# Kernel optimization log

Measured on AMD Instinct MI355X. Metric: run time of the kernel, lower is better.

Reference implementation:

```python
import jax, jax.numpy as jnp
import numpy as np

N, E, C, EC, L = 50000, 600000, 128, 16, 4
LN_EPS = 1e-5


def setup_inputs() -> dict:
    key = jax.random.key(0)
    ks = jax.random.split(key, 10)
    return {
        "x": jax.random.normal(ks[0], (N, C), jnp.float32),
        "edge_attr": jax.random.normal(ks[1], (E, EC), jnp.float32),
        "We": jax.random.normal(ks[2], (EC, C), jnp.float32) / np.sqrt(EC).astype(np.float32),
        "be": jnp.zeros((C,), jnp.float32),
        "W1": jax.random.normal(ks[3], (L, C, C), jnp.float32) / np.sqrt(C).astype(np.float32),
        "b1": jnp.zeros((L, C), jnp.float32),
        "W2": jax.random.normal(ks[4], (L, C, C), jnp.float32) / np.sqrt(C).astype(np.float32),
        "b2": jnp.zeros((L, C), jnp.float32),
        "gamma": jnp.ones((L, C), jnp.float32),
        "beta": jnp.zeros((L, C), jnp.float32),
        "edge_index": jax.random.randint(ks[5], (2, E), 0, N, dtype=jnp.int32),
    }


def reference(x, edge_attr, We, be, W1, b1, W2, b2, gamma, beta, edge_index):
    src = edge_index[0]  # x_j (message source)
    dst = edge_index[1]  # aggregation target
    # lin_edge: Linear + SiLU, shared across layers
    ea = jax.nn.silu(edge_attr @ We + be)  # [E, C]
    n = x.shape[0]
    for l in range(L):
        # GINEConv message: ReLU(x_j + edge_attr), scatter-sum to target nodes
        msg = jax.nn.relu(x[src] + ea)                       # [E, C]
        agg = jax.ops.segment_sum(msg, dst, num_segments=n)  # [N, C]
        h = x + agg  # (1 + eps) * x + agg, eps = 0
        # GINEConv nn: Linear -> SiLU -> Linear
        h = jax.nn.silu(h @ W1[l] + b1[l]) @ W2[l] + b2[l]
        # residual + LayerNorm
        y = x + h
        mu = y.mean(-1, keepdims=True)
        var = y.var(-1, keepdims=True)
        x = (y - mu) * jax.lax.rsqrt(var + LN_EPS) * gamma[l] + beta[l]
    return x
```

## Files before the change

kernel.cpp:

```cpp
#include <hip/hip_runtime.h>

#define NN 50000
#define EE 600000
#define CC 128
#define ECC 16
#define LL 4
#define LN_EPS 1e-5f
#define MTILE 80
#define PADC 136
#define YSTR 132

typedef float f32x4 __attribute__((ext_vector_type(4)));
typedef short bf16x8 __attribute__((ext_vector_type(8)));

static __device__ __forceinline__ float bf2f(unsigned short u) {
  union { unsigned int i; float f; } v; v.i = ((unsigned int)u) << 16; return v.f;
}
static __device__ __forceinline__ unsigned short f2bf(float f) {
  union { float f; unsigned int i; } v; v.f = f;
  unsigned int b = v.i + 0x7FFFu + ((v.i >> 16) & 1u);
  return (unsigned short)(b >> 16);
}
static __device__ __forceinline__ unsigned pk2bf(float lo, float hi) {
  unsigned r;
  asm("v_cvt_pk_bf16_f32 %0, %1, %2" : "=v"(r) : "v"(lo), "v"(hi));
  return r;
}
static __device__ __forceinline__ float silu_f(float v) {
  return v * __builtin_amdgcn_rcpf(1.f + __expf(-v));
}


__global__ void count_kernel(const int* __restrict__ dst, int* __restrict__ counts, int E) {
  int e = blockIdx.x * blockDim.x + threadIdx.x;
  if (e < E) atomicAdd(&counts[dst[e]], 1);
}

__global__ __launch_bounds__(1024) void scan1_kernel(const int* __restrict__ counts,
                                                     int* __restrict__ bsum, int n) {
  __shared__ int wsum[16];
  const int tid = threadIdx.x, lane = tid & 63, wv = tid >> 6;
  const int i = blockIdx.x * 1024 + tid;
  int s = (i < n) ? counts[i] : 0;
  #pragma unroll
  for (int off = 1; off < 64; off <<= 1) s += __shfl_xor(s, off);
  if (lane == 0) wsum[wv] = s;
  __syncthreads();
  if (tid == 0) {
    int t = 0;
    #pragma unroll
    for (int j = 0; j < 16; ++j) t += wsum[j];
    bsum[blockIdx.x] = t;
  }
}

__global__ void scan2_kernel(const int* __restrict__ bsum, int* __restrict__ boff, int nb) {
  const int lane = threadIdx.x;
  int v = (lane < nb) ? bsum[lane] : 0;
  int incl = v;
  #pragma unroll
  for (int off = 1; off < 64; off <<= 1) {
    int t = __shfl_up(incl, off);
    if (lane >= off) incl += t;
  }
  if (lane < nb) boff[lane] = incl - v;
}

__global__ __launch_bounds__(1024) void scan3_kernel(const int* __restrict__ counts,
                                                     const int* __restrict__ boff,
                                                     int* __restrict__ rowptr, int n) {
  __shared__ int wsum[16];
  const int tid = threadIdx.x, lane = tid & 63, wv = tid >> 6;
  const int i = blockIdx.x * 1024 + tid;
  const int v = (i < n) ? counts[i] : 0;
  int incl = v;
  #pragma unroll
  for (int off = 1; off < 64; off <<= 1) {
    int t = __shfl_up(incl, off);
    if (lane >= off) incl += t;
  }
  if (lane == 63) wsum[wv] = incl;
  __syncthreads();
  if (wv == 0) {
    int vv = (lane < 16) ? wsum[lane] : 0;
    int vi = vv;
    #pragma unroll
    for (int off = 1; off < 16; off <<= 1) {
      int t = __shfl_up(vi, off);
      if (lane >= off) vi += t;
    }
    if (lane < 16) wsum[lane] = vi - vv;
  }
  __syncthreads();
  if (i < n) rowptr[i + 1] = boff[blockIdx.x] + wsum[wv] + incl;
  if (i == 0) rowptr[0] = 0;
}

__global__ void fill_kernel(const int* __restrict__ src, const int* __restrict__ dst,
                            const int* __restrict__ rowptr, int* __restrict__ cursor,
                            int* __restrict__ eidx, int* __restrict__ esrc, int E) {
  int e = blockIdx.x * blockDim.x + threadIdx.x;
  if (e < E) {
    const int d = dst[e];
    const int pos = rowptr[d] + atomicAdd(&cursor[d], 1);
    eidx[pos] = e;
    esrc[pos] = src[e];
  }
}


__global__ __launch_bounds__(256) void xconv_kernel(const float* __restrict__ x,
                                                    unsigned short* __restrict__ xb) {
  const int t = blockIdx.x * 256 + threadIdx.x;
  if (t >= NN * CC / 8) return;
  const float4 a = ((const float4*)x)[t * 2];
  const float4 b = ((const float4*)x)[t * 2 + 1];
  uint4 o;
  o.x = pk2bf(a.x, a.y);
  o.y = pk2bf(a.z, a.w);
  o.z = pk2bf(b.x, b.y);
  o.w = pk2bf(b.z, b.w);
  ((uint4*)xb)[t] = o;
}


__global__ void webconv_kernel(const float* __restrict__ We, unsigned short* __restrict__ webf) {
  const int t = blockIdx.x * blockDim.x + threadIdx.x;
  if (t >= 8 * 64 * 8) return;
  const int j = t & 7, l = (t >> 3) & 63, cg = t >> 9;
  const int k = (l >> 4) * 8 + j, c = cg * 16 + (l & 15);
  webf[t] = (k < 16) ? f2bf(We[k * CC + c]) : (unsigned short)0;
}


__global__ __launch_bounds__(256) void ea_kernel(const float* __restrict__ edge_attr,
                                                 const unsigned short* __restrict__ webf,
                                                 const float* __restrict__ be,
                                                 const int* __restrict__ eidx,
                                                 unsigned short* __restrict__ ea) {
  __shared__ float er[64][20];
  __shared__ unsigned short eaT[64 * 132];
  const int tid = threadIdx.x;
  const int lane = tid & 63, wv = tid >> 6;

  bf16x8 bw[8];
  #pragma unroll
  for (int cg = 0; cg < 8; ++cg)
    bw[cg] = *(const bf16x8*)(webf + cg * 512 + lane * 8);
  float bev[8];
  #pragma unroll
  for (int cg = 0; cg < 8; ++cg) bev[cg] = be[cg * 16 + (lane & 15)];

  const int base = blockIdx.x * 64;
  {
    const int r = tid >> 2, q = tid & 3;
    const int e = eidx[base + r];
    *(float4*)(&er[r][q * 4]) = *(const float4*)(edge_attr + (size_t)e * ECC + q * 4);
  }
  __syncthreads();

  const int arow = wv * 16 + (lane & 15);
  const int ko = lane >> 4;
  union { unsigned short u[8]; unsigned v32[4]; bf16x8 v; } afu;
  if (ko < 2) {
    const float* ep = &er[arow][ko * 8];
    afu.v32[0] = pk2bf(ep[0], ep[1]);
    afu.v32[1] = pk2bf(ep[2], ep[3]);
    afu.v32[2] = pk2bf(ep[4], ep[5]);
    afu.v32[3] = pk2bf(ep[6], ep[7]);
  } else {
    #pragma unroll
    for (int j = 0; j < 4; ++j) afu.v32[j] = 0;
  }

  f32x4 acc[8];
  #pragma unroll
  for (int cg = 0; cg < 8; ++cg) {
    acc[cg] = (f32x4)0.f;
    acc[cg] = __builtin_amdgcn_mfma_f32_16x16x32_bf16(afu.v, bw[cg], acc[cg], 0, 0, 0);
  }

  const int rl0 = wv * 16 + ko * 4;
  const int cb = lane & 15;
  #pragma unroll
  for (int cg = 0; cg < 8; cg += 2)
    #pragma unroll
    for (int r = 0; r < 4; ++r) {
      const float v0 = silu_f(acc[cg][r] + bev[cg]);
      const float v1 = silu_f(acc[cg + 1][r] + bev[cg + 1]);
      const unsigned pk = pk2bf(v0, v1);
      unsigned short* rp = &eaT[(rl0 + r) * 132 + cb];
      rp[cg * 16]       = (unsigned short)pk;
      rp[(cg + 1) * 16] = (unsigned short)(pk >> 16);
    }
  __syncthreads();

  uint4* eg = (uint4*)(ea + (size_t)base * CC);
  #pragma unroll
  for (int k = 0; k < 4; ++k) {
    const int u = tid + k * 256;
    const int row = u >> 4, ch = u & 15;
    eg[u] = *(const uint4*)(&eaT[row * 132 + ch * 8]);
  }
}


__global__ __launch_bounds__(128) void wconv_kernel(const float* __restrict__ W1,
                                                    const float* __restrict__ W2,
                                                    unsigned short* __restrict__ wt) {
  const int b = blockIdx.x;
  const int c = b & (CC - 1);
  const int mat = (b >> 7) & 1;
  const int l = b >> 8;
  const float* W = (mat ? W2 : W1) + (size_t)l * CC * CC;
  unsigned short* o = wt + ((size_t)l * 2 + mat) * CC * CC + (size_t)c * CC;
  const int k = threadIdx.x;
  o[k] = f2bf(W[(size_t)k * CC + c]);
}


__global__ __launch_bounds__(256) void agg4_kernel(const unsigned short* __restrict__ xb,
                                                   unsigned short* __restrict__ h_out,
                                                   const unsigned short* __restrict__ ea,
                                                   const int* __restrict__ rowptr,
                                                   const int* __restrict__ esrc) {
  const int tid = threadIdx.x;
  const int lane = tid & 63;
  const int half = lane >> 5;
  const int l32 = lane & 31;
  const int c0 = l32 * 4;
  const int wv = tid >> 6;
  const int n = blockIdx.x * 4 + wv;

  const int p0 = rowptr[n], p1 = rowptr[n + 1];
  float a0 = 0.f, a1 = 0.f, a2 = 0.f, a3 = 0.f;

  int p = p0 + half;
  for (; p + 6 < p1; p += 8) {
    const int s0 = esrc[p], s1 = esrc[p + 2], s2 = esrc[p + 4], s3 = esrc[p + 6];
    const uint2 x0 = *(const uint2*)(xb + (size_t)s0 * CC + c0);
    const uint2 x1 = *(const uint2*)(xb + (size_t)s1 * CC + c0);
    const uint2 x2 = *(const uint2*)(xb + (size_t)s2 * CC + c0);
    const uint2 x3 = *(const uint2*)(xb + (size_t)s3 * CC + c0);
    const uint2 e0 = *(const uint2*)(ea + (size_t)p * CC + c0);
    const uint2 e1 = *(const uint2*)(ea + (size_t)(p + 2) * CC + c0);
    const uint2 e2 = *(const uint2*)(ea + (size_t)(p + 4) * CC + c0);
    const uint2 e3 = *(const uint2*)(ea + (size_t)(p + 6) * CC + c0);
    a0 += fmaxf(bf2f((unsigned short)x0.x) + bf2f((unsigned short)e0.x), 0.f)
        + fmaxf(bf2f((unsigned short)x1.x) + bf2f((unsigned short)e1.x), 0.f)
        + fmaxf(bf2f((unsigned short)x2.x) + bf2f((unsigned short)e2.x), 0.f)
        + fmaxf(bf2f((unsigned short)x3.x) + bf2f((unsigned short)e3.x), 0.f);
    a1 += fmaxf(bf2f((unsigned short)(x0.x >> 16)) + bf2f((unsigned short)(e0.x >> 16)), 0.f)
        + fmaxf(bf2f((unsigned short)(x1.x >> 16)) + bf2f((unsigned short)(e1.x >> 16)), 0.f)
        + fmaxf(bf2f((unsigned short)(x2.x >> 16)) + bf2f((unsigned short)(e2.x >> 16)), 0.f)
        + fmaxf(bf2f((unsigned short)(x3.x >> 16)) + bf2f((unsigned short)(e3.x >> 16)), 0.f);
    a2 += fmaxf(bf2f((unsigned short)x0.y) + bf2f((unsigned short)e0.y), 0.f)
        + fmaxf(bf2f((unsigned short)x1.y) + bf2f((unsigned short)e1.y), 0.f)
        + fmaxf(bf2f((unsigned short)x2.y) + bf2f((unsigned short)e2.y), 0.f)
        + fmaxf(bf2f((unsigned short)x3.y) + bf2f((unsigned short)e3.y), 0.f);
    a3 += fmaxf(bf2f((unsigned short)(x0.y >> 16)) + bf2f((unsigned short)(e0.y >> 16)), 0.f)
        + fmaxf(bf2f((unsigned short)(x1.y >> 16)) + bf2f((unsigned short)(e1.y >> 16)), 0.f)
        + fmaxf(bf2f((unsigned short)(x2.y >> 16)) + bf2f((unsigned short)(e2.y >> 16)), 0.f)
        + fmaxf(bf2f((unsigned short)(x3.y >> 16)) + bf2f((unsigned short)(e3.y >> 16)), 0.f);
  }
  for (; p < p1; p += 2) {
    const int s0 = esrc[p];
    const uint2 x0 = *(const uint2*)(xb + (size_t)s0 * CC + c0);
    const uint2 e0 = *(const uint2*)(ea + (size_t)p * CC + c0);
    a0 += fmaxf(bf2f((unsigned short)x0.x) + bf2f((unsigned short)e0.x), 0.f);
    a1 += fmaxf(bf2f((unsigned short)(x0.x >> 16)) + bf2f((unsigned short)(e0.x >> 16)), 0.f);
    a2 += fmaxf(bf2f((unsigned short)x0.y) + bf2f((unsigned short)e0.y), 0.f);
    a3 += fmaxf(bf2f((unsigned short)(x0.y >> 16)) + bf2f((unsigned short)(e0.y >> 16)), 0.f);
  }

  a0 += __shfl_xor(a0, 32);
  a1 += __shfl_xor(a1, 32);
  a2 += __shfl_xor(a2, 32);
  a3 += __shfl_xor(a3, 32);

  if (half == 0) {
    const uint2 xs = *(const uint2*)(xb + (size_t)n * CC + c0);
    uint2 pk;
    pk.x = pk2bf(bf2f((unsigned short)xs.x) + a0, bf2f((unsigned short)(xs.x >> 16)) + a1);
    pk.y = pk2bf(bf2f((unsigned short)xs.y) + a2, bf2f((unsigned short)(xs.y >> 16)) + a3);
    *(uint2*)(h_out + (size_t)n * CC + c0) = pk;
  }
}


__global__ __launch_bounds__(256) void agg_fb_kernel(const unsigned short* __restrict__ xb,
                                                     unsigned short* __restrict__ h_out,
                                                     const float* __restrict__ edge_attr,
                                                     const float* __restrict__ We,
                                                     const float* __restrict__ be,
                                                     const int* __restrict__ rowptr,
                                                     const int* __restrict__ eidx,
                                                     const int* __restrict__ esrc) {
  const int tid = threadIdx.x;
  const int c = tid & (CC - 1);
  const int g = tid >> 7;
  const int n = blockIdx.x * 2 + g;

  float wec[ECC];
  #pragma unroll
  for (int k = 0; k < ECC; ++k) wec[k] = We[k * CC + c];
  const float bev = be[c];

  const int p0 = rowptr[n], p1 = rowptr[n + 1];
  float acc = 0.f;
  for (int p = p0; p < p1; ++p) {
    const int e0 = eidx[p];
    const int s0 = esrc[p];
    const float4* ar0 = (const float4*)(edge_attr + (size_t)e0 * ECC);
    const float4 a0 = ar0[0], a1 = ar0[1], a2 = ar0[2], a3 = ar0[3];
    float v0 = bev
      + a0.x*wec[0]  + a0.y*wec[1]  + a0.z*wec[2]  + a0.w*wec[3]
      + a1.x*wec[4]  + a1.y*wec[5]  + a1.z*wec[6]  + a1.w*wec[7]
      + a2.x*wec[8]  + a2.y*wec[9]  + a2.z*wec[10] + a2.w*wec[11]
      + a3.x*wec[12] + a3.y*wec[13] + a3.z*wec[14] + a3.w*wec[15];
    acc += fmaxf(bf2f(xb[(size_t)s0 * CC + c]) + silu_f(v0), 0.f);
  }
  h_out[(size_t)n * CC + c] = f2bf(bf2f(xb[(size_t)n * CC + c]) + acc);
}


template <int FINAL>
__global__ __launch_bounds__(256) void mlp_kernel(unsigned short* xb,
                                                  const unsigned short* __restrict__ hbuf,
                                                  const unsigned short* __restrict__ wt1,
                                                  const unsigned short* __restrict__ wt2,
                                                  const float* __restrict__ b1,
                                                  const float* __restrict__ b2,
                                                  const float* __restrict__ gamma,
                                                  const float* __restrict__ beta,
                                                  float* __restrict__ out) {
  __shared__ __align__(16) char smem[MTILE * PADC * 2 * 2];
  unsigned short* hA = (unsigned short*)smem;
  unsigned short* tA = (unsigned short*)(smem + MTILE * PADC * 2);
  float* yS = (float*)smem;
  __shared__ float red[MTILE][4][2];

  const int tid = threadIdx.x;
  const int lane = tid & 63;
  const int wv = tid >> 6;
  const int node0 = blockIdx.x * MTILE;
  const int colq = lane & 15;
  const int krow = lane >> 4;
  const int colb = wv * 32;

  for (int idx = tid; idx < MTILE * 16; idx += 256) {
    const int row = idx >> 4, ch = idx & 15;
    *(uint4*)(&hA[row * PADC + ch * 8]) =
        *(const uint4*)(hbuf + (size_t)(node0 + row) * CC + ch * 8);
  }
  __syncthreads();

  bf16x8 bw[2][4];
  #pragma unroll
  for (int n2 = 0; n2 < 2; ++n2)
    #pragma unroll
    for (int kk = 0; kk < 4; ++kk)
      bw[n2][kk] = *(const bf16x8*)(wt1 + (size_t)(colb + n2 * 16 + colq) * CC + kk * 32 + krow * 8);

  f32x4 acc[5][2];
  #pragma unroll
  for (int m = 0; m < 5; ++m) { acc[m][0] = (f32x4)0.f; acc[m][1] = (f32x4)0.f; }

  #pragma unroll
  for (int m = 0; m < 5; ++m)
    #pragma unroll
    for (int kk = 0; kk < 4; ++kk) {
      const bf16x8 a = *(const bf16x8*)(&hA[(m * 16 + colq) * PADC + kk * 32 + krow * 8]);
      acc[m][0] = __builtin_amdgcn_mfma_f32_16x16x32_bf16(a, bw[0][kk], acc[m][0], 0, 0, 0);
      acc[m][1] = __builtin_amdgcn_mfma_f32_16x16x32_bf16(a, bw[1][kk], acc[m][1], 0, 0, 0);
    }

  const float b1v0 = b1[colb + colq], b1v1 = b1[colb + 16 + colq];
  #pragma unroll
  for (int m = 0; m < 5; ++m)
    #pragma unroll
    for (int r = 0; r < 4; ++r) {
      const int row = m * 16 + krow * 4 + r;
      const unsigned pk = pk2bf(silu_f(acc[m][0][r] + b1v0), silu_f(acc[m][1][r] + b1v1));
      tA[row * PADC + colb + colq]      = (unsigned short)pk;
      tA[row * PADC + colb + 16 + colq] = (unsigned short)(pk >> 16);
    }
  __syncthreads();

  #pragma unroll
  for (int n2 = 0; n2 < 2; ++n2)
    #pragma unroll
    for (int kk = 0; kk < 4; ++kk)
      bw[n2][kk] = *(const bf16x8*)(wt2 + (size_t)(colb + n2 * 16 + colq) * CC + kk * 32 + krow * 8);

  f32x4 acc2[5][2];
  #pragma unroll
  for (int m = 0; m < 5; ++m) { acc2[m][0] = (f32x4)0.f; acc2[m][1] = (f32x4)0.f; }

  #pragma unroll
  for (int m = 0; m < 5; ++m)
    #pragma unroll
    for (int kk = 0; kk < 4; ++kk) {
      const bf16x8 a = *(const bf16x8*)(&tA[(m * 16 + colq) * PADC + kk * 32 + krow * 8]);
      acc2[m][0] = __builtin_amdgcn_mfma_f32_16x16x32_bf16(a, bw[0][kk], acc2[m][0], 0, 0, 0);
      acc2[m][1] = __builtin_amdgcn_mfma_f32_16x16x32_bf16(a, bw[1][kk], acc2[m][1], 0, 0, 0);
    }

  const float b2v0 = b2[colb + colq], b2v1 = b2[colb + 16 + colq];
  float yv[5][2][4];
  #pragma unroll
  for (int m = 0; m < 5; ++m)
    #pragma unroll
    for (int r = 0; r < 4; ++r) {
      const int row = m * 16 + krow * 4 + r;
      yv[m][0][r] = acc2[m][0][r] + b2v0 + bf2f(xb[(size_t)(node0 + row) * CC + colb + colq]);
      yv[m][1][r] = acc2[m][1][r] + b2v1 + bf2f(xb[(size_t)(node0 + row) * CC + colb + 16 + colq]);
    }

  #pragma unroll
  for (int m = 0; m < 5; ++m)
    #pragma unroll
    for (int r = 0; r < 4; ++r) {
      float s = yv[m][0][r] + yv[m][1][r];
      float s2 = yv[m][0][r] * yv[m][0][r] + yv[m][1][r] * yv[m][1][r];
      #pragma unroll
      for (int off = 1; off < 16; off <<= 1) {
        s  += __shfl_xor(s, off);
        s2 += __shfl_xor(s2, off);
      }
      if (colq == 0) {
        const int row = m * 16 + krow * 4 + r;
        red[row][wv][0] = s;
        red[row][wv][1] = s2;
      }
    }
  __syncthreads();

  const float gm0 = gamma[colb + colq], gm1 = gamma[colb + 16 + colq];
  const float bt0 = beta[colb + colq],  bt1 = beta[colb + 16 + colq];
  #pragma unroll
  for (int m = 0; m < 5; ++m)
    #pragma unroll
    for (int r = 0; r < 4; ++r) {
      const int row = m * 16 + krow * 4 + r;
      const float s  = red[row][0][0] + red[row][1][0] + red[row][2][0] + red[row][3][0];
      const float s2 = red[row][0][1] + red[row][1][1] + red[row][2][1] + red[row][3][1];
      const float mean = s * (1.f / 128.f);
      const float var = s2 * (1.f / 128.f) - mean * mean;
      const float rstd = rsqrtf(var + LN_EPS);
      yS[row * YSTR + colb + colq]      = (yv[m][0][r] - mean) * rstd * gm0 + bt0;
      yS[row * YSTR + colb + 16 + colq] = (yv[m][1][r] - mean) * rstd * gm1 + bt1;
    }
  __syncthreads();

  if (FINAL) {
    float* og = out + (size_t)node0 * CC;
    #pragma unroll
    for (int k = 0; k < 10; ++k) {
      const int u = tid + k * 256;
      const int row = u >> 5, q = u & 31;
      *(float4*)(og + u * 4) = *(const float4*)(&yS[row * YSTR + q * 4]);
    }
  } else {
    unsigned short* xg = xb + (size_t)node0 * CC;
    #pragma unroll
    for (int k = 0; k < 5; ++k) {
      const int u = tid + k * 256;
      const int row = u >> 4, ch8 = u & 15;
      const float* yp = &yS[row * YSTR + ch8 * 8];
      uint4 o;
      o.x = pk2bf(yp[0], yp[1]);
      o.y = pk2bf(yp[2], yp[3]);
      o.z = pk2bf(yp[4], yp[5]);
      o.w = pk2bf(yp[6], yp[7]);
      *(uint4*)(xg + u * 8) = o;
    }
  }
}


extern "C" void kernel_launch(void* const* d_in, const int* in_sizes, int n_in,
                              void* d_out, int out_size, void* d_ws, size_t ws_size,
                              hipStream_t stream) {
  const float* x         = (const float*)d_in[0];
  const float* edge_attr = (const float*)d_in[1];
  const float* We        = (const float*)d_in[2];
  const float* be        = (const float*)d_in[3];
  const float* W1        = (const float*)d_in[4];
  const float* b1        = (const float*)d_in[5];
  const float* W2        = (const float*)d_in[6];
  const float* b2        = (const float*)d_in[7];
  const float* gamma     = (const float*)d_in[8];
  const float* beta      = (const float*)d_in[9];
  const int*   ei        = (const int*)d_in[10];
  const int*   src       = ei;
  const int*   dst       = ei + EE;
  float* out = (float*)d_out;

  char* ws = (char*)d_ws;
  unsigned short* xbf    = (unsigned short*)(ws + 0);
  unsigned short* hbuf   = (unsigned short*)(ws + 12800000);
  unsigned short* wt     = (unsigned short*)(ws + 25600000);
  int*            counts = (int*)(ws + 25862400);
  int*            rowptr = (int*)(ws + 26062592);
  int*            cursor = (int*)(ws + 26262784);
  int*            eidx   = (int*)(ws + 26462976);
  int*            esrc   = (int*)(ws + 28863232);
  unsigned short* ea     = (unsigned short*)(ws + 31263360);
  unsigned short* webf   = (unsigned short*)(ws + 26262784);
  int*            bsum   = (int*)(ws + 26462976);
  int*            boff   = (int*)(ws + 26462976 + 256);
  const bool use_ea = (ws_size >= 184863360ull);
  const int NB = (NN + 1023) / 1024;

  hipMemsetAsync(counts, 0, (size_t)NN * 4, stream);
  hipMemsetAsync(cursor, 0, (size_t)NN * 4, stream);
  count_kernel<<<(EE + 255) / 256, 256, 0, stream>>>(dst, counts, EE);
  scan1_kernel<<<NB, 1024, 0, stream>>>(counts, bsum, NN);
  scan2_kernel<<<1, 64, 0, stream>>>(bsum, boff, NB);
  scan3_kernel<<<NB, 1024, 0, stream>>>(counts, boff, rowptr, NN);
  fill_kernel<<<(EE + 255) / 256, 256, 0, stream>>>(src, dst, rowptr, cursor, eidx, esrc, EE);
  wconv_kernel<<<LL * 2 * CC, 128, 0, stream>>>(W1, W2, wt);
  xconv_kernel<<<(NN * CC / 8 + 255) / 256, 256, 0, stream>>>(x, xbf);
  if (use_ea) {
    webconv_kernel<<<16, 256, 0, stream>>>(We, webf);
    ea_kernel<<<EE / 64, 256, 0, stream>>>(edge_attr, webf, be, eidx, ea);
  }

  for (int l = 0; l < LL; ++l) {
    if (use_ea)
      agg4_kernel<<<NN / 4, 256, 0, stream>>>(xbf, hbuf, ea, rowptr, esrc);
    else
      agg_fb_kernel<<<NN / 2, 256, 0, stream>>>(xbf, hbuf, edge_attr, We, be, rowptr, eidx, esrc);
    const unsigned short* w1p = wt + ((size_t)l * 2) * CC * CC;
    const unsigned short* w2p = wt + ((size_t)l * 2 + 1) * CC * CC;
    const float* b1p = b1 + (size_t)l * CC;
    const float* b2p = b2 + (size_t)l * CC;
    const float* gmp = gamma + (size_t)l * CC;
    const float* btp = beta + (size_t)l * CC;
    if (l == LL - 1)
      mlp_kernel<1><<<NN / MTILE, 256, 0, stream>>>(xbf, hbuf, w1p, w2p, b1p, b2p, gmp, btp, out);
    else
      mlp_kernel<0><<<NN / MTILE, 256, 0, stream>>>(xbf, hbuf, w1p, w2p, b1p, b2p, gmp, btp, out);
  }
}
```

Measured before the change: 408.1 us.

## Fuse edge-feature MLP recompute into per-layer aggregation with MFMA

Drops the precomputed bf16 edge-embedding buffer (E×C) and its producer kernel. Each layer now runs a fused aggregation kernel that handles a tile of 16 destination nodes. It stages their incoming edges' raw attributes and gathered source rows in shared memory, recomputes SiLU(edge_attr@We+be) with MFMA, forms the ReLU messages, and reduces them serially per channel into the node outputs. This replaces a large write plus four large reads of the edge-embedding buffer with small reads of the 16-wide attributes and some recompute. The costs are extra block-level synchronisation, a serial per-channel reduction loop run by only half the threads, and higher shared-memory use per block.

```diff
diff --git a/kernel.cpp b/kernel.cpp
--- a/kernel.cpp
+++ b/kernel.cpp
@@ -9,6 +9,8 @@
 #define MTILE 80
 #define PADC 136
 #define YSTR 132
+#define NTB 16
+#define EB 64
 
 typedef float f32x4 __attribute__((ext_vector_type(4)));
 typedef short bf16x8 __attribute__((ext_vector_type(8)));
@@ -133,78 +135,6 @@
 }
 
 
-__global__ __launch_bounds__(256) void ea_kernel(const float* __restrict__ edge_attr,
-                                                 const unsigned short* __restrict__ webf,
-                                                 const float* __restrict__ be,
-                                                 const int* __restrict__ eidx,
-                                                 unsigned short* __restrict__ ea) {
-  __shared__ float er[64][20];
-  __shared__ unsigned short eaT[64 * 132];
-  const int tid = threadIdx.x;
-  const int lane = tid & 63, wv = tid >> 6;
-
-  bf16x8 bw[8];
-  #pragma unroll
-  for (int cg = 0; cg < 8; ++cg)
-    bw[cg] = *(const bf16x8*)(webf + cg * 512 + lane * 8);
-  float bev[8];
-  #pragma unroll
-  for (int cg = 0; cg < 8; ++cg) bev[cg] = be[cg * 16 + (lane & 15)];
-
-  const int base = blockIdx.x * 64;
-  {
-    const int r = tid >> 2, q = tid & 3;
-    const int e = eidx[base + r];
-    *(float4*)(&er[r][q * 4]) = *(const float4*)(edge_attr + (size_t)e * ECC + q * 4);
-  }
-  __syncthreads();
-
-  const int arow = wv * 16 + (lane & 15);
-  const int ko = lane >> 4;
-  union { unsigned short u[8]; unsigned v32[4]; bf16x8 v; } afu;
-  if (ko < 2) {
-    const float* ep = &er[arow][ko * 8];
-    afu.v32[0] = pk2bf(ep[0], ep[1]);
-    afu.v32[1] = pk2bf(ep[2], ep[3]);
-    afu.v32[2] = pk2bf(ep[4], ep[5]);
-    afu.v32[3] = pk2bf(ep[6], ep[7]);
-  } else {
-    #pragma unroll
-    for (int j = 0; j < 4; ++j) afu.v32[j] = 0;
-  }
-
-  f32x4 acc[8];
-  #pragma unroll
-  for (int cg = 0; cg < 8; ++cg) {
-    acc[cg] = (f32x4)0.f;
-    acc[cg] = __builtin_amdgcn_mfma_f32_16x16x32_bf16(afu.v, bw[cg], acc[cg], 0, 0, 0);
-  }
-
-  const int rl0 = wv * 16 + ko * 4;
-  const int cb = lane & 15;
-  #pragma unroll
-  for (int cg = 0; cg < 8; cg += 2)
-    #pragma unroll
-    for (int r = 0; r < 4; ++r) {
-      const float v0 = silu_f(acc[cg][r] + bev[cg]);
-      const float v1 = silu_f(acc[cg + 1][r] + bev[cg + 1]);
-      const unsigned pk = pk2bf(v0, v1);
-      unsigned short* rp = &eaT[(rl0 + r) * 132 + cb];
-      rp[cg * 16]       = (unsigned short)pk;
-      rp[(cg + 1) * 16] = (unsigned short)(pk >> 16);
-    }
-  __syncthreads();
-
-  uint4* eg = (uint4*)(ea + (size_t)base * CC);
-  #pragma unroll
-  for (int k = 0; k < 4; ++k) {
-    const int u = tid + k * 256;
-    const int row = u >> 4, ch = u & 15;
-    eg[u] = *(const uint4*)(&eaT[row * 132 + ch * 8]);
-  }
-}
-
-
 __global__ __launch_bounds__(128) void wconv_kernel(const float* __restrict__ W1,
                                                     const float* __restrict__ W2,
                                                     unsigned short* __restrict__ wt) {
@@ -219,108 +149,116 @@
 }
 
 
-__global__ __launch_bounds__(256) void agg4_kernel(const unsigned short* __restrict__ xb,
+__global__ __launch_bounds__(256) void fagg_kernel(const unsigned short* __restrict__ xb,
                                                    unsigned short* __restrict__ h_out,
-                                                   const unsigned short* __restrict__ ea,
+                                                   const float* __restrict__ edge_attr,
+                                                   const unsigned short* __restrict__ webf,
+                                                   const float* __restrict__ be,
                                                    const int* __restrict__ rowptr,
+                                                   const int* __restrict__ eidx,
                                                    const int* __restrict__ esrc) {
+  __shared__ float er[EB][20];
+  __shared__ unsigned short xT[EB * 132];
+  __shared__ unsigned short msgT[EB * 132];
+  __shared__ int rp[NTB + 1];
+
   const int tid = threadIdx.x;
-  const int lane = tid & 63;
-  const int half = lane >> 5;
-  const int l32 = lane & 31;
-  const int c0 = l32 * 4;
-  const int wv = tid >> 6;
-  const int n = blockIdx.x * 4 + wv;
-
-  const int p0 = rowptr[n], p1 = rowptr[n + 1];
-  float a0 = 0.f, a1 = 0.f, a2 = 0.f, a3 = 0.f;
-
-  int p = p0 + half;
-  for (; p + 6 < p1; p += 8) {
-    const int s0 = esrc[p], s1 = esrc[p + 2], s2 = esrc[p + 4], s3 = esrc[p + 6];
-    const uint2 x0 = *(const uint2*)(xb + (size_t)s0 * CC + c0);
-    const uint2 x1 = *(const uint2*)(xb + (size_t)s1 * CC + c0);
-    const uint2 x2 = *(const uint2*)(xb + (size_t)s2 * CC + c0);
-    const uint2 x3 = *(const uint2*)(xb + (size_t)s3 * CC + c0);
-    const uint2 e0 = *(const uint2*)(ea + (size_t)p * CC + c0);
-    const uint2 e1 = *(const uint2*)(ea + (size_t)(p + 2) * CC + c0);
-    const uint2 e2 = *(const uint2*)(ea + (size_t)(p + 4) * CC + c0);
-    const uint2 e3 = *(const uint2*)(ea + (size_t)(p + 6) * CC + c0);
-    a0 += fmaxf(bf2f((unsigned short)x0.x) + bf2f((unsigned short)e0.x), 0.f)
-        + fmaxf(bf2f((unsigned short)x1.x) + bf2f((unsigned short)e1.x), 0.f)
-        + fmaxf(bf2f((unsigned short)x2.x) + bf2f((unsigned short)e2.x), 0.f)
-        + fmaxf(bf2f((unsigned short)x3.x) + bf2f((unsigned short)e3.x), 0.f);
-    a1 += fmaxf(bf2f((unsigned short)(x0.x >> 16)) + bf2f((unsigned short)(e0.x >> 16)), 0.f)
-        + fmaxf(bf2f((unsigned short)(x1.x >> 16)) + bf2f((unsigned short)(e1.x >> 16)), 0.f)
-        + fmaxf(bf2f((unsigned short)(x2.x >> 16)) + bf2f((unsigned short)(e2.x >> 16)), 0.f)
-        + fmaxf(bf2f((unsigned short)(x3.x >> 16)) + bf2f((unsigned short)(e3.x >> 16)), 0.f);
-    a2 += fmaxf(bf2f((unsigned short)x0.y) + bf2f((unsigned short)e0.y), 0.f)
-        + fmaxf(bf2f((unsigned short)x1.y) + bf2f((unsigned short)e1.y), 0.f)
-        + fmaxf(bf2f((unsigned short)x2.y) + bf2f((unsigned short)e2.y), 0.f)
-        + fmaxf(bf2f((unsigned short)x3.y) + bf2f((unsigned short)e3.y), 0.f);
-    a3 += fmaxf(bf2f((unsigned short)(x0.y >> 16)) + bf2f((unsigned short)(e0.y >> 16)), 0.f)
-        + fmaxf(bf2f((unsigned short)(x1.y >> 16)) + bf2f((unsigned short)(e1.y >> 16)), 0.f)
-        + fmaxf(bf2f((unsigned short)(x2.y >> 16)) + bf2f((unsigned short)(e2.y >> 16)), 0.f)
-        + fmaxf(bf2f((unsigned short)(x3.y >> 16)) + bf2f((unsigned short)(e3.y >> 16)), 0.f);
-  }
-  for (; p < p1; p += 2) {
-    const int s0 = esrc[p];
-    const uint2 x0 = *(const uint2*)(xb + (size_t)s0 * CC + c0);
-    const uint2 e0 = *(const uint2*)(ea + (size_t)p * CC + c0);
-    a0 += fmaxf(bf2f((unsigned short)x0.x) + bf2f((unsigned short)e0.x), 0.f);
-    a1 += fmaxf(bf2f((unsigned short)(x0.x >> 16)) + bf2f((unsigned short)(e0.x >> 16)), 0.f);
-    a2 += fmaxf(bf2f((unsigned short)x0.y) + bf2f((unsigned short)e0.y), 0.f);
-    a3 += fmaxf(bf2f((unsigned short)(x0.y >> 16)) + bf2f((unsigned short)(e0.y >> 16)), 0.f);
-  }
-
-  a0 += __shfl_xor(a0, 32);
-  a1 += __shfl_xor(a1, 32);
-  a2 += __shfl_xor(a2, 32);
-  a3 += __shfl_xor(a3, 32);
-
-  if (half == 0) {
-    const uint2 xs = *(const uint2*)(xb + (size_t)n * CC + c0);
-    uint2 pk;
-    pk.x = pk2bf(bf2f((unsigned short)xs.x) + a0, bf2f((unsigned short)(xs.x >> 16)) + a1);
-    pk.y = pk2bf(bf2f((unsigned short)xs.y) + a2, bf2f((unsigned short)(xs.y >> 16)) + a3);
-    *(uint2*)(h_out + (size_t)n * CC + c0) = pk;
-  }
-}
-
-
-__global__ __launch_bounds__(256) void agg_fb_kernel(const unsigned short* __restrict__ xb,
-                                                     unsigned short* __restrict__ h_out,
-                                                     const float* __restrict__ edge_attr,
-                                                     const float* __restrict__ We,
-                                                     const float* __restrict__ be,
-                                                     const int* __restrict__ rowptr,
-                                                     const int* __restrict__ eidx,
-                                                     const int* __restrict__ esrc) {
-  const int tid = threadIdx.x;
-  const int c = tid & (CC - 1);
-  const int g = tid >> 7;
-  const int n = blockIdx.x * 2 + g;
-
-  float wec[ECC];
-  #pragma unroll
-  for (int k = 0; k < ECC; ++k) wec[k] = We[k * CC + c];
-  const float bev = be[c];
-
-  const int p0 = rowptr[n], p1 = rowptr[n + 1];
-  float acc = 0.f;
-  for (int p = p0; p < p1; ++p) {
-    const int e0 = eidx[p];
-    const int s0 = esrc[p];
-    const float4* ar0 = (const float4*)(edge_attr + (size_t)e0 * ECC);
-    const float4 a0 = ar0[0], a1 = ar0[1], a2 = ar0[2], a3 = ar0[3];
-    float v0 = bev
-      + a0.x*wec[0]  + a0.y*wec[1]  + a0.z*wec[2]  + a0.w*wec[3]
-      + a1.x*wec[4]  + a1.y*wec[5]  + a1.z*wec[6]  + a1.w*wec[7]
-      + a2.x*wec[8]  + a2.y*wec[9]  + a2.z*wec[10] + a2.w*wec[11]
-      + a3.x*wec[12] + a3.y*wec[13] + a3.z*wec[14] + a3.w*wec[15];
-    acc += fmaxf(bf2f(xb[(size_t)s0 * CC + c]) + silu_f(v0), 0.f);
-  }
-  h_out[(size_t)n * CC + c] = f2bf(bf2f(xb[(size_t)n * CC + c]) + acc);
+  const int lane = tid & 63, wv = tid >> 6;
+  const int l16 = lane & 15, ko = lane >> 4;
+  const int node0 = blockIdx.x * NTB;
+
+  if (tid <= NTB) rp[tid] = rowptr[node0 + tid];
+
+  bf16x8 bw[8];
+  #pragma unroll
+  for (int cg = 0; cg < 8; ++cg)
+    bw[cg] = *(const bf16x8*)(webf + cg * 512 + lane * 8);
+  float bev[8];
+  #pragma unroll
+  for (int cg = 0; cg < 8; ++cg) bev[cg] = be[cg * 16 + l16];
+
+  __syncthreads();
+  const int p0 = rp[0], p1 = rp[NTB];
+
+  const int c = tid;
+  int ni = 0;
+  int nxt = rp[1];
+  float accv = 0.f;
+
+  const int gr = tid >> 2, gq = tid & 3;
+
+  for (int pb = p0; pb < p1; pb += EB) {
+    const int nb = min(EB, p1 - pb);
+
+    if (gr < nb) {
+      const int p = pb + gr;
+      const int e = eidx[p];
+      *(float4*)(&er[gr][gq * 4]) = *(const float4*)(edge_attr + (size_t)e * ECC + gq * 4);
+      const int s = esrc[p];
+      const uint4* xr = (const uint4*)(xb + (size_t)s * CC + gq * 32);
+      uint4* xd = (uint4*)(&xT[gr * 132 + gq * 32]);
+      xd[0] = xr[0]; xd[1] = xr[1]; xd[2] = xr[2]; xd[3] = xr[3];
+    }
+    __syncthreads();
+
+    union { unsigned v32[4]; bf16x8 v; } af;
+    const int arow = wv * 16 + l16;
+    if (ko < 2 && arow < nb) {
+      const float* ep = &er[arow][ko * 8];
+      af.v32[0] = pk2bf(ep[0], ep[1]);
+      af.v32[1] = pk2bf(ep[2], ep[3]);
+      af.v32[2] = pk2bf(ep[4], ep[5]);
+      af.v32[3] = pk2bf(ep[6], ep[7]);
+    } else {
+      af.v32[0] = af.v32[1] = af.v32[2] = af.v32[3] = 0;
+    }
+    f32x4 acc[8];
+    #pragma unroll
+    for (int cg = 0; cg < 8; ++cg) {
+      acc[cg] = (f32x4)0.f;
+      acc[cg] = __builtin_amdgcn_mfma_f32_16x16x32_bf16(af.v, bw[cg], acc[cg], 0, 0, 0);
+    }
+
+    const int rl0 = wv * 16 + ko * 4;
+    #pragma unroll
+    for (int cg = 0; cg < 8; cg += 2)
+      #pragma unroll
+      for (int r = 0; r < 4; ++r) {
+        const int row = rl0 + r;
+        const float e0 = silu_f(acc[cg][r] + bev[cg]);
+        const float e1 = silu_f(acc[cg + 1][r] + bev[cg + 1]);
+        const float x0 = bf2f(xT[row * 132 + cg * 16 + l16]);
+        const float x1 = bf2f(xT[row * 132 + (cg + 1) * 16 + l16]);
+        const unsigned pk = pk2bf(fmaxf(x0 + e0, 0.f), fmaxf(x1 + e1, 0.f));
+        msgT[row * 132 + cg * 16 + l16]       = (unsigned short)pk;
+        msgT[row * 132 + (cg + 1) * 16 + l16] = (unsigned short)(pk >> 16);
+      }
+    __syncthreads();
+
+    if (tid < 128) {
+      for (int r = 0; r < nb; ++r) {
+        const int p = pb + r;
+        while (p >= nxt && ni < NTB - 1) {
+          const int n = node0 + ni;
+          h_out[(size_t)n * CC + c] = f2bf(bf2f(xb[(size_t)n * CC + c]) + accv);
+          accv = 0.f;
+          ++ni;
+          nxt = rp[ni + 1];
+        }
+        accv += bf2f(msgT[r * 132 + c]);
+      }
+    }
+    __syncthreads();
+  }
+
+  if (tid < 128) {
+    const int n = node0 + ni;
+    h_out[(size_t)n * CC + c] = f2bf(bf2f(xb[(size_t)n * CC + c]) + accv);
+    for (int k = ni + 1; k < NTB; ++k) {
+      const int nn = node0 + k;
+      h_out[(size_t)nn * CC + c] = xb[(size_t)nn * CC + c];
+    }
+  }
 }
 
 
@@ -506,11 +444,9 @@
   int*            cursor = (int*)(ws + 26262784);
   int*            eidx   = (int*)(ws + 26462976);
   int*            esrc   = (int*)(ws + 28863232);
-  unsigned short* ea     = (unsigned short*)(ws + 31263360);
   unsigned short* webf   = (unsigned short*)(ws + 26262784);
   int*            bsum   = (int*)(ws + 26462976);
   int*            boff   = (int*)(ws + 26462976 + 256);
-  const bool use_ea = (ws_size >= 184863360ull);
   const int NB = (NN + 1023) / 1024;
 
   hipMemsetAsync(counts, 0, (size_t)NN * 4, stream);
@@ -522,16 +458,11 @@
   fill_kernel<<<(EE + 255) / 256, 256, 0, stream>>>(src, dst, rowptr, cursor, eidx, esrc, EE);
   wconv_kernel<<<LL * 2 * CC, 128, 0, stream>>>(W1, W2, wt);
   xconv_kernel<<<(NN * CC / 8 + 255) / 256, 256, 0, stream>>>(x, xbf);
-  if (use_ea) {
-    webconv_kernel<<<16, 256, 0, stream>>>(We, webf);
-    ea_kernel<<<EE / 64, 256, 0, stream>>>(edge_attr, webf, be, eidx, ea);
-  }
+  webconv_kernel<<<16, 256, 0, stream>>>(We, webf);
 
   for (int l = 0; l < LL; ++l) {
-    if (use_ea)
-      agg4_kernel<<<NN / 4, 256, 0, stream>>>(xbf, hbuf, ea, rowptr, esrc);
-    else
-      agg_fb_kernel<<<NN / 2, 256, 0, stream>>>(xbf, hbuf, edge_attr, We, be, rowptr, eidx, esrc);
+    fagg_kernel<<<NN / NTB, 256, 0, stream>>>(xbf, hbuf, edge_attr, webf, be,
+                                              rowptr, eidx, esrc);
     const unsigned short* w1p = wt + ((size_t)l * 2) * CC * CC;
     const unsigned short* w2p = wt + ((size_t)l * 2 + 1) * CC * CC;
     const float* b1p = b1 + (size_t)l * CC;
```

After: 639.4 us. 56.7% more time.
